# Kernel tuning notes

Hardware: AMD Instinct MI355X
Metric: run time of the kernel (lower is better)

The kernel has to match this reference:

```python
import jax, jax.numpy as jnp
import numpy as np

B, T, D, H, K = 8, 4096, 768, 12, 64
EPS_WKV = 1e-9
EPS_GN = 1e-5


def setup_inputs() -> dict:
    key = jax.random.key(0)
    ks = jax.random.split(key, 12)
    x = jax.random.normal(ks[0], (B, T, D), jnp.float32)
    # linear projection weights (torch nn.Linear stores [out, in]; y = x @ W.T)
    W_r = jax.random.normal(ks[1], (D, D), jnp.float32) * 0.02
    W_k = jax.random.normal(ks[2], (D, D), jnp.float32) * 0.02
    W_v = jax.random.normal(ks[3], (D, D), jnp.float32) * 0.02
    W_o = jax.random.normal(ks[4], (D, D), jnp.float32) * 0.02
    time_mix_r = jax.random.uniform(ks[5], (D,), jnp.float32)
    time_mix_k = jax.random.uniform(ks[6], (D,), jnp.float32)
    time_mix_v = jax.random.uniform(ks[7], (D,), jnp.float32)
    # around the module's init values (time_decay ~ -0.075, time_first ~ 0.15 at layer 6/12)
    time_decay = -0.075 + 0.1 * jax.random.normal(ks[8], (H, K), jnp.float32)
    time_first = 0.15 + 0.1 * jax.random.normal(ks[9], (H, K), jnp.float32)
    gn_weight = jnp.ones((D,), jnp.float32)
    gn_bias = jnp.zeros((D,), jnp.float32)
    return {
        "x": x,
        "time_mix_r": time_mix_r, "time_mix_k": time_mix_k, "time_mix_v": time_mix_v,
        "time_decay": time_decay, "time_first": time_first,
        "W_r": W_r, "W_k": W_k, "W_v": W_v, "W_o": W_o,
        "gn_weight": gn_weight, "gn_bias": gn_bias,
    }


def reference(x, time_mix_r, time_mix_k, time_mix_v, time_decay, time_first,
              W_r, W_k, W_v, W_o, gn_weight, gn_bias):
    Bx, Tx, Dx = x.shape
    Hx, Kx = time_decay.shape
    # token-shift: previous timestep (zero-initialized state)
    x_prev = jnp.concatenate([jnp.zeros_like(x[:, :1]), x[:, :-1]], axis=1)
    xr = x * time_mix_r + x_prev * (1.0 - time_mix_r)
    xk = x * time_mix_k + x_prev * (1.0 - time_mix_k)
    xv = x * time_mix_v + x_prev * (1.0 - time_mix_v)
    r = jax.nn.sigmoid(xr @ W_r.T).reshape(Bx, Tx, Hx, Kx)
    k = (xk @ W_k.T).reshape(Bx, Tx, Hx, Kx)
    v = (xv @ W_v.T).reshape(Bx, Tx, Hx, Kx)

    w = jnp.exp(-jnp.exp(time_decay))   # [H,K] decay per channel
    eu = jnp.exp(time_first)            # [H,K] bonus for current token

    def step(carry, kv_t):
        num, den = carry                # each [B,H,K]
        k_t, v_t = kv_t                 # each [B,H,K]
        ek = jnp.exp(k_t)
        wkv = (num + eu * ek * v_t) / (den + eu * ek + EPS_WKV)
        return (num * w + ek * v_t, den * w + ek), wkv

    k_tm = jnp.moveaxis(k, 1, 0)        # [T,B,H,K]
    v_tm = jnp.moveaxis(v, 1, 0)
    init = (jnp.zeros((Bx, Hx, Kx), x.dtype), jnp.zeros((Bx, Hx, Kx), x.dtype))
    _, wkv = jax.lax.scan(step, init, (k_tm, v_tm))
    out = jnp.moveaxis(wkv, 0, 1)       # [B,T,H,K]

    y = r * out                         # [B,T,H,K]
    # torch GroupNorm(H, D) on [B, D, T]: normalize each group over (K channels x T steps)
    mean = y.mean(axis=(1, 3), keepdims=True)
    var = y.var(axis=(1, 3), keepdims=True)
    y = (y - mean) * jax.lax.rsqrt(var + EPS_GN)
    y = y * gn_weight.reshape(1, 1, Hx, Kx) + gn_bias.reshape(1, 1, Hx, Kx)
    return y.reshape(Bx, Tx, Dx) @ W_o.T
```

## Files before the change

kernel.cpp:

```cpp
#include <hip/hip_runtime.h>
#include <hip/hip_bf16.h>
#include <cstdint>

#define B_ 8
#define T_ 4096
#define D_ 768
#define H_ 12
#define M_ (B_*T_)
#define CHUNKS 256
#define CLEN 16
#define WELEM (D_*D_)
#define NCH (B_*H_*64)

typedef __attribute__((ext_vector_type(8))) short bf16x8;
typedef __attribute__((ext_vector_type(4))) float f32x4;

static __device__ __forceinline__ unsigned short f2bf(float f) {
  __hip_bfloat16 h = __float2bfloat16(f);
  return __builtin_bit_cast(unsigned short, h);
}
static __device__ __forceinline__ float bf2f(unsigned short u) {
  unsigned v = ((unsigned)u) << 16;
  return __builtin_bit_cast(float, v);
}

static __device__ __forceinline__ void async16(const void* g, void* l) {
  __builtin_amdgcn_global_load_lds(
      (const __attribute__((address_space(1))) unsigned int*)g,
      (__attribute__((address_space(3))) unsigned int*)l, 16, 0, 0);
}

__global__ __launch_bounds__(256) void zero_out_kernel(float* __restrict__ out, size_t n4) {
  size_t gid = (size_t)blockIdx.x * 256 + threadIdx.x;
  if (gid < n4) *(float4*)(out + gid * 4) = make_float4(0.f, 0.f, 0.f, 0.f);
}

__global__ __launch_bounds__(256) void mix_kernel(
    const float* __restrict__ x, const float* __restrict__ tmr,
    const float* __restrict__ tmk, const float* __restrict__ tmv,
    unsigned short* __restrict__ xr, unsigned short* __restrict__ xk,
    unsigned short* __restrict__ xv) {
  size_t gid = (size_t)blockIdx.x * 256 + threadIdx.x;
  size_t idx4 = gid * 4;
  int d = (int)(idx4 % D_);
  size_t row = idx4 / D_;
  int t = (int)(row & (T_ - 1));
  float4 xc = *(const float4*)(x + idx4);
  float4 xp = make_float4(0.f, 0.f, 0.f, 0.f);
  if (t > 0) xp = *(const float4*)(x + idx4 - D_);
  float4 mr = *(const float4*)(tmr + d);
  float4 mk = *(const float4*)(tmk + d);
  float4 mv = *(const float4*)(tmv + d);
  ushort4 orr, okk, ovv;
  orr.x = f2bf(xc.x*mr.x + xp.x*(1.f-mr.x));
  orr.y = f2bf(xc.y*mr.y + xp.y*(1.f-mr.y));
  orr.z = f2bf(xc.z*mr.z + xp.z*(1.f-mr.z));
  orr.w = f2bf(xc.w*mr.w + xp.w*(1.f-mr.w));
  okk.x = f2bf(xc.x*mk.x + xp.x*(1.f-mk.x));
  okk.y = f2bf(xc.y*mk.y + xp.y*(1.f-mk.y));
  okk.z = f2bf(xc.z*mk.z + xp.z*(1.f-mk.z));
  okk.w = f2bf(xc.w*mk.w + xp.w*(1.f-mk.w));
  ovv.x = f2bf(xc.x*mv.x + xp.x*(1.f-mv.x));
  ovv.y = f2bf(xc.y*mv.y + xp.y*(1.f-mv.y));
  ovv.z = f2bf(xc.z*mv.z + xp.z*(1.f-mv.z));
  ovv.w = f2bf(xc.w*mv.w + xp.w*(1.f-mv.w));
  *(ushort4*)(xr + idx4) = orr;
  *(ushort4*)(xk + idx4) = okk;
  *(ushort4*)(xv + idx4) = ovv;
}

__global__ __launch_bounds__(256) void wconv_kernel(
    const float* __restrict__ a, const float* __restrict__ b,
    const float* __restrict__ c, const float* __restrict__ d,
    unsigned short* __restrict__ o) {
  size_t gid = (size_t)blockIdx.x * 256 + threadIdx.x;
  size_t idx4 = gid * 4;
  size_t mi = idx4 / WELEM;
  size_t off = idx4 % WELEM;
  const float* src = (mi == 0) ? a : (mi == 1) ? b : (mi == 2) ? c : d;
  float4 v = *(const float4*)(src + off);
  ushort4 u;
  u.x = f2bf(v.x); u.y = f2bf(v.y); u.z = f2bf(v.z); u.w = f2bf(v.w);
  *(ushort4*)(o + idx4) = u;
}

template<int ACT, int OBF>
__global__ __launch_bounds__(256) void gemm_nt(
    const unsigned short* __restrict__ A,
    const unsigned short* __restrict__ Bw,
    void* __restrict__ Cv, int M, int N, int Kd) {
  __shared__ __align__(16) unsigned short smem[128 * 128];
  unsigned short* As = smem;
  unsigned short* Bs = smem + 128 * 64;
  const int tid = threadIdx.x;
  const int wave = tid >> 6, lane = tid & 63;
  const int quad = lane >> 4, l16 = lane & 15;

  int nwg = gridDim.x * gridDim.y;
  int lin = blockIdx.y * gridDim.x + blockIdx.x;
  int q = nwg >> 3, r = nwg & 7;
  int xcd = lin & 7, off = lin >> 3;
  int swz = (xcd < r ? xcd * (q + 1) : r * (q + 1) + (xcd - r) * q) + off;
  const int m0 = (swz / gridDim.x) * 128;
  const int n0 = (swz % gridDim.x) * 128;
  const int wm = (wave & 1) * 64, wn = (wave >> 1) * 64;

  f32x4 acc[4][4] = {};

  for (int kb = 0; kb < Kd; kb += 64) {
    __syncthreads();
#pragma unroll
    for (int j = 0; j < 4; ++j) {
      int chunk = j * 256 + tid;
      int row = chunk >> 3, slot = chunk & 7;
      int ks = slot ^ (row & 7);
      async16(A  + ((size_t)(m0 + row) * Kd + kb + ks * 8), &As[chunk * 8]);
      async16(Bw + ((size_t)(n0 + row) * Kd + kb + ks * 8), &Bs[chunk * 8]);
    }
    __syncthreads();

#pragma unroll
    for (int kk = 0; kk < 2; ++kk) {
      bf16x8 a[4], b[4];
#pragma unroll
      for (int i = 0; i < 4; ++i) {
        int ra = wm + i * 16 + l16;
        a[i] = *(const bf16x8*)&As[ra * 64 + (((kk * 4 + quad) ^ (ra & 7)) * 8)];
        int rb = wn + i * 16 + l16;
        b[i] = *(const bf16x8*)&Bs[rb * 64 + (((kk * 4 + quad) ^ (rb & 7)) * 8)];
      }
#pragma unroll
      for (int i = 0; i < 4; ++i)
#pragma unroll
        for (int jj = 0; jj < 4; ++jj)
          acc[i][jj] = __builtin_amdgcn_mfma_f32_16x16x32_bf16(a[i], b[jj], acc[i][jj], 0, 0, 0);
    }
  }

  if (OBF) {
    __syncthreads();
    unsigned short* Cs = smem;
#pragma unroll
    for (int i = 0; i < 4; ++i) {
#pragma unroll
      for (int jj = 0; jj < 4; ++jj) {
        int col = wn + jj * 16 + l16;
#pragma unroll
        for (int rr = 0; rr < 4; ++rr) {
          int row = wm + i * 16 + quad * 4 + rr;
          float v = acc[i][jj][rr];
          if (ACT == 1) v = 1.f / (1.f + __expf(-v));
          int cg = (col >> 3) ^ (row & 7);
          Cs[row * 128 + cg * 8 + (col & 7)] = f2bf(v);
        }
      }
    }
    __syncthreads();
#pragma unroll
    for (int g = 0; g < 8; ++g) {
      int gi = g * 256 + tid;
      int row = gi >> 4, cg = gi & 15;
      int sg = cg ^ (row & 7);
      bf16x8 vv = *(const bf16x8*)&Cs[row * 128 + sg * 8];
      *(bf16x8*)((unsigned short*)Cv + (size_t)(m0 + row) * N + n0 + cg * 8) = vv;
    }
  } else {
#pragma unroll
    for (int i = 0; i < 4; ++i) {
      int rowb = m0 + wm + i * 16 + quad * 4;
#pragma unroll
      for (int jj = 0; jj < 4; ++jj) {
        int col = n0 + wn + jj * 16 + l16;
#pragma unroll
        for (int rr = 0; rr < 4; ++rr) {
          float v = acc[i][jj][rr];
          ((float*)Cv)[(size_t)(rowb + rr) * N + col] = v;
        }
      }
    }
  }
}

__global__ __launch_bounds__(256) void wkv_pass1(
    const unsigned short* __restrict__ Kb, const unsigned short* __restrict__ Vb,
    const float* __restrict__ td,
    float* __restrict__ sumN, float* __restrict__ sumD) {
  int gid = blockIdx.x * 256 + threadIdx.x;
  int kg = gid & 7;
  int tmp = gid >> 3;
  int h = tmp % H_;
  tmp /= H_;
  int b = tmp % B_;
  int c = tmp / B_;
  const float* tdp = td + h * 64 + kg * 8;
  float w[8], num[8], den[8];
#pragma unroll
  for (int j = 0; j < 8; ++j) {
    w[j] = __expf(-__expf(tdp[j]));
    num[j] = 0.f; den[j] = 0.f;
  }
  size_t base = ((size_t)(b * T_ + c * CLEN)) * D_ + h * 64 + kg * 8;
#pragma unroll 4
  for (int i = 0; i < CLEN; ++i) {
    bf16x8 k8 = *(const bf16x8*)(Kb + base + (size_t)i * D_);
    bf16x8 v8 = *(const bf16x8*)(Vb + base + (size_t)i * D_);
#pragma unroll
    for (int j = 0; j < 8; ++j) {
      float ek = __expf(bf2f((unsigned short)k8[j]));
      num[j] = num[j] * w[j] + ek * bf2f((unsigned short)v8[j]);
      den[j] = den[j] * w[j] + ek;
    }
  }
  int ob = ((c * B_ + b) * H_ + h) * 64 + kg * 8;
  *(float4*)(sumN + ob)     = make_float4(num[0], num[1], num[2], num[3]);
  *(float4*)(sumN + ob + 4) = make_float4(num[4], num[5], num[6], num[7]);
  *(float4*)(sumD + ob)     = make_float4(den[0], den[1], den[2], den[3]);
  *(float4*)(sumD + ob + 4) = make_float4(den[4], den[5], den[6], den[7]);
}

__global__ __launch_bounds__(256) void wkv_pass2(
    const float* __restrict__ sumN, const float* __restrict__ sumD,
    const float* __restrict__ td,
    float* __restrict__ prefN, float* __restrict__ prefD,
    float* __restrict__ gstats) {
  int tid = blockIdx.x * 256 + threadIdx.x;
  if (blockIdx.x == 0 && threadIdx.x < 192) gstats[threadIdx.x] = 0.f;
  int k = tid & 63;
  int h = (tid >> 6) % H_;
  float w = __expf(-__expf(td[h * 64 + k]));
  float wL = w;
#pragma unroll
  for (int i = 0; i < 4; ++i) wL *= wL;
  float n = 0.f, d = 0.f;
  for (int c = 0; c < CHUNKS; ++c) {
    int j = c * NCH + tid;
    prefN[j] = n; prefD[j] = d;
    n = n * wL + sumN[j];
    d = d * wL + sumD[j];
  }
}

__global__ __launch_bounds__(256) void wkv_pass3(
    const unsigned short* __restrict__ Kb, const unsigned short* __restrict__ Vb,
    unsigned short* __restrict__ RY,
    const float* __restrict__ td, const float* __restrict__ tf,
    const float* __restrict__ prefN, const float* __restrict__ prefD,
    float* __restrict__ gsum, float* __restrict__ gsq) {
  int gid = blockIdx.x * 256 + threadIdx.x;
  int kg = gid & 7;
  int tmp = gid >> 3;
  int h = tmp % H_;
  tmp /= H_;
  int b = tmp % B_;
  int c = tmp / B_;
  const float* tdp = td + h * 64 + kg * 8;
  const float* tfp = tf + h * 64 + kg * 8;
  float w[8], eu[8], num[8], den[8];
  int sb = ((c * B_ + b) * H_ + h) * 64 + kg * 8;
  float4 n0 = *(const float4*)(prefN + sb), n1 = *(const float4*)(prefN + sb + 4);
  float4 d0 = *(const float4*)(prefD + sb), d1 = *(const float4*)(prefD + sb + 4);
  num[0]=n0.x; num[1]=n0.y; num[2]=n0.z; num[3]=n0.w;
  num[4]=n1.x; num[5]=n1.y; num[6]=n1.z; num[7]=n1.w;
  den[0]=d0.x; den[1]=d0.y; den[2]=d0.z; den[3]=d0.w;
  den[4]=d1.x; den[5]=d1.y; den[6]=d1.z; den[7]=d1.w;
#pragma unroll
  for (int j = 0; j < 8; ++j) {
    w[j]  = __expf(-__expf(tdp[j]));
    eu[j] = __expf(tfp[j]);
  }
  size_t base = ((size_t)(b * T_ + c * CLEN)) * D_ + h * 64 + kg * 8;
  float s1 = 0.f, s2 = 0.f;
#pragma unroll 4
  for (int i = 0; i < CLEN; ++i) {
    size_t idx = base + (size_t)i * D_;
    bf16x8 k8 = *(const bf16x8*)(Kb + idx);
    bf16x8 v8 = *(const bf16x8*)(Vb + idx);
    bf16x8 r8 = *(const bf16x8*)(RY + idx);
    bf16x8 y8;
#pragma unroll
    for (int j = 0; j < 8; ++j) {
      float kk = bf2f((unsigned short)k8[j]);
      float vv = bf2f((unsigned short)v8[j]);
      float rr = bf2f((unsigned short)r8[j]);
      float ek = __expf(kk);
      float wkv = (num[j] + eu[j] * ek * vv) / (den[j] + eu[j] * ek + 1e-9f);
      unsigned short ybf = f2bf(rr * wkv);
      y8[j] = (short)ybf;
      float y = bf2f(ybf);
      s1 += y; s2 += y * y;
      num[j] = num[j] * w[j] + ek * vv;
      den[j] = den[j] * w[j] + ek;
    }
    *(bf16x8*)(RY + idx) = y8;
  }
#pragma unroll
  for (int off = 4; off; off >>= 1) {
    s1 += __shfl_xor(s1, off);
    s2 += __shfl_xor(s2, off);
  }
  if (kg == 0) {
    atomicAdd(&gsum[b * H_ + h], s1);
    atomicAdd(&gsq [b * H_ + h], s2);
  }
}

__global__ __launch_bounds__(256) void gn_kernel(
    const unsigned short* __restrict__ Y, const float* __restrict__ gsum,
    const float* __restrict__ gsq, const float* __restrict__ gw,
    const float* __restrict__ gb, unsigned short* __restrict__ Ybf) {
  size_t gid = (size_t)blockIdx.x * 256 + threadIdx.x;
  size_t idx4 = gid * 4;
  int d = (int)(idx4 % D_);
  size_t row = idx4 / D_;
  int b = (int)(row >> 12);
  int h = d >> 6;
  int g = b * H_ + h;
  const float inv = 1.f / (float)(T_ * 64);
  float mean = gsum[g] * inv;
  float var = gsq[g] * inv - mean * mean;
  float rstd = rsqrtf(var + 1e-5f);
  ushort4 yu = *(const ushort4*)(Y + idx4);
  float4 wv = *(const float4*)(gw + d);
  float4 bv = *(const float4*)(gb + d);
  ushort4 o;
  o.x = f2bf((bf2f(yu.x) - mean) * rstd * wv.x + bv.x);
  o.y = f2bf((bf2f(yu.y) - mean) * rstd * wv.y + bv.y);
  o.z = f2bf((bf2f(yu.z) - mean) * rstd * wv.z + bv.z);
  o.w = f2bf((bf2f(yu.w) - mean) * rstd * wv.w + bv.w);
  *(ushort4*)(Ybf + idx4) = o;
}

extern "C" void kernel_launch(void* const* d_in, const int* in_sizes, int n_in,
                              void* d_out, int out_size, void* d_ws, size_t ws_size,
                              hipStream_t stream) {
  (void)in_sizes; (void)n_in;
  const float* x   = (const float*)d_in[0];
  const float* tmr = (const float*)d_in[1];
  const float* tmk = (const float*)d_in[2];
  const float* tmv = (const float*)d_in[3];
  const float* td  = (const float*)d_in[4];
  const float* tf  = (const float*)d_in[5];
  const float* Wr  = (const float*)d_in[6];
  const float* Wk  = (const float*)d_in[7];
  const float* Wv  = (const float*)d_in[8];
  const float* Wo  = (const float*)d_in[9];
  const float* gw  = (const float*)d_in[10];
  const float* gb  = (const float*)d_in[11];
  float* out = (float*)d_out;

  constexpr size_t MD = (size_t)M_ * D_;
  constexpr size_t NEED = 4 * (MD * 2)
                        + (size_t)4 * WELEM * 2
                        + 4 * ((size_t)CHUNKS * NCH * 4)
                        + 1024;
  if (ws_size < NEED) {
    zero_out_kernel<<<(int)((MD / 4 + 255) / 256), 256, 0, stream>>>(out, MD / 4);
    return;
  }

  char* ws = (char*)d_ws;
  unsigned short* XR = (unsigned short*)ws; ws += MD * 2;
  unsigned short* XK = (unsigned short*)ws; ws += MD * 2;
  unsigned short* XV = (unsigned short*)ws; ws += MD * 2;
  unsigned short* Rb = (unsigned short*)ws; ws += MD * 2;
  unsigned short* Wb = (unsigned short*)ws; ws += (size_t)4 * WELEM * 2;
  float* sumN  = (float*)ws; ws += (size_t)CHUNKS * NCH * 4;
  float* sumD  = (float*)ws; ws += (size_t)CHUNKS * NCH * 4;
  float* prefN = (float*)ws; ws += (size_t)CHUNKS * NCH * 4;
  float* prefD = (float*)ws; ws += (size_t)CHUNKS * NCH * 4;
  float* gstats = (float*)ws; ws += 1024;
  unsigned short* Kb = XR;
  unsigned short* Vb = XK;
  unsigned short* Yb = XV;

  mix_kernel<<<(int)(MD / 1024), 256, 0, stream>>>(x, tmr, tmk, tmv, XR, XK, XV);
  wconv_kernel<<<(4 * WELEM / 4) / 256, 256, 0, stream>>>(Wr, Wk, Wv, Wo, Wb);

  dim3 ggrid(D_ / 128, M_ / 128);
  gemm_nt<1, 1><<<ggrid, 256, 0, stream>>>(XR, Wb,             Rb, M_, D_, D_);
  gemm_nt<0, 1><<<ggrid, 256, 0, stream>>>(XK, Wb + WELEM,     Kb, M_, D_, D_);
  gemm_nt<0, 1><<<ggrid, 256, 0, stream>>>(XV, Wb + 2 * WELEM, Vb, M_, D_, D_);

  wkv_pass1<<<(CHUNKS * NCH / 8) / 256, 256, 0, stream>>>(Kb, Vb, td, sumN, sumD);
  wkv_pass2<<<NCH / 256, 256, 0, stream>>>(sumN, sumD, td, prefN, prefD, gstats);
  wkv_pass3<<<(CHUNKS * NCH / 8) / 256, 256, 0, stream>>>(Kb, Vb, Rb, td, tf,
                                                          prefN, prefD, gstats, gstats + 96);
  gn_kernel<<<(int)(MD / 1024), 256, 0, stream>>>(Rb, gstats, gstats + 96, gw, gb, Yb);

  gemm_nt<0, 0><<<ggrid, 256, 0, stream>>>(Yb, Wb + 3 * WELEM, out, M_, D_, D_);
}
```

Measured before the change: 538.3 us.

## Multi-stage pipeline GEMM loads, parallelize chunk prefix scan, use fast divide

Result: no change. 538.6 us (+0.1%).

```diff
diff --git a/kernel.cpp b/kernel.cpp
--- a/kernel.cpp
+++ b/kernel.cpp
@@ -89,9 +89,7 @@
     const unsigned short* __restrict__ A,
     const unsigned short* __restrict__ Bw,
     void* __restrict__ Cv, int M, int N, int Kd) {
-  __shared__ __align__(16) unsigned short smem[128 * 128];
-  unsigned short* As = smem;
-  unsigned short* Bs = smem + 128 * 64;
+  __shared__ __align__(16) unsigned short smem[4][128 * 64];
   const int tid = threadIdx.x;
   const int wave = tid >> 6, lane = tid & 63;
   const int quad = lane >> 4, l16 = lane & 15;
@@ -105,41 +103,48 @@
   const int n0 = (swz % gridDim.x) * 128;
   const int wm = (wave & 1) * 64, wn = (wave >> 1) * 64;
 
-  f32x4 acc[4][4] = {};
-
-  for (int kb = 0; kb < Kd; kb += 64) {
-    __syncthreads();
-#pragma unroll
-    for (int j = 0; j < 4; ++j) {
+  auto stage = [&](int buf, int kb) {
+    unsigned short* As = smem[buf];
+    unsigned short* Bs = smem[buf] + 128 * 32;
+#pragma unroll
+    for (int j = 0; j < 2; ++j) {
       int chunk = j * 256 + tid;
-      int row = chunk >> 3, slot = chunk & 7;
-      int ks = slot ^ (row & 7);
+      int row = chunk >> 2, slot = chunk & 3;
+      int ks = slot ^ ((row >> 1) & 3);
       async16(A  + ((size_t)(m0 + row) * Kd + kb + ks * 8), &As[chunk * 8]);
       async16(Bw + ((size_t)(n0 + row) * Kd + kb + ks * 8), &Bs[chunk * 8]);
     }
-    __syncthreads();
-
-#pragma unroll
-    for (int kk = 0; kk < 2; ++kk) {
-      bf16x8 a[4], b[4];
-#pragma unroll
-      for (int i = 0; i < 4; ++i) {
-        int ra = wm + i * 16 + l16;
-        a[i] = *(const bf16x8*)&As[ra * 64 + (((kk * 4 + quad) ^ (ra & 7)) * 8)];
-        int rb = wn + i * 16 + l16;
-        b[i] = *(const bf16x8*)&Bs[rb * 64 + (((kk * 4 + quad) ^ (rb & 7)) * 8)];
-      }
-#pragma unroll
-      for (int i = 0; i < 4; ++i)
-#pragma unroll
-        for (int jj = 0; jj < 4; ++jj)
-          acc[i][jj] = __builtin_amdgcn_mfma_f32_16x16x32_bf16(a[i], b[jj], acc[i][jj], 0, 0, 0);
-    }
+  };
+
+  f32x4 acc[4][4] = {};
+  const int NT = Kd >> 5;
+
+  stage(0, 0); stage(1, 32); stage(2, 64);
+  for (int t = 0; t < NT; ++t) {
+    if (t < NT - 2)       asm volatile("s_waitcnt vmcnt(8)" ::: "memory");
+    else if (t == NT - 2) asm volatile("s_waitcnt vmcnt(4)" ::: "memory");
+    else                  asm volatile("s_waitcnt vmcnt(0)" ::: "memory");
+    __builtin_amdgcn_s_barrier();
+    if (t + 3 < NT) stage((t + 3) & 3, (t + 3) * 32);
+    const unsigned short* As = smem[t & 3];
+    const unsigned short* Bs = smem[t & 3] + 128 * 32;
+    bf16x8 a[4], b[4];
+#pragma unroll
+    for (int i = 0; i < 4; ++i) {
+      int ra = wm + i * 16 + l16;
+      a[i] = *(const bf16x8*)&As[ra * 32 + ((quad ^ ((ra >> 1) & 3)) * 8)];
+      int rb = wn + i * 16 + l16;
+      b[i] = *(const bf16x8*)&Bs[rb * 32 + ((quad ^ ((rb >> 1) & 3)) * 8)];
+    }
+#pragma unroll
+    for (int i = 0; i < 4; ++i)
+#pragma unroll
+      for (int jj = 0; jj < 4; ++jj)
+        acc[i][jj] = __builtin_amdgcn_mfma_f32_16x16x32_bf16(a[i], b[jj], acc[i][jj], 0, 0, 0);
   }
 
   if (OBF) {
-    __syncthreads();
-    unsigned short* Cs = smem;
+    unsigned short* Cs = (unsigned short*)smem;
 #pragma unroll
     for (int i = 0; i < 4; ++i) {
 #pragma unroll
@@ -223,20 +228,49 @@
     const float* __restrict__ td,
     float* __restrict__ prefN, float* __restrict__ prefD,
     float* __restrict__ gstats) {
-  int tid = blockIdx.x * 256 + threadIdx.x;
-  if (blockIdx.x == 0 && threadIdx.x < 192) gstats[threadIdx.x] = 0.f;
-  int k = tid & 63;
-  int h = (tid >> 6) % H_;
-  float w = __expf(-__expf(td[h * 64 + k]));
+  __shared__ float tile[256][64];
+  int bid = blockIdx.x;
+  if (bid == 0 && threadIdx.x < 192) gstats[threadIdx.x] = 0.f;
+  int bh = bid >> 1, qd = bid & 1;
+  const float* src = qd ? sumD : sumN;
+  float* dst = qd ? prefD : prefN;
+  int h = bh % H_;
+  int base = bh * 64;
+  int t = threadIdx.x;
+  {
+    int c4 = (t & 15) * 4;
+    int rg = t >> 4;
+#pragma unroll 4
+    for (int i = 0; i < 16; ++i) {
+      int row = rg * 16 + i;
+      *(float4*)&tile[row][c4] = *(const float4*)&src[(size_t)row * NCH + base + c4];
+    }
+  }
+  __syncthreads();
+  int ch = t & 63, g = t >> 6;
+  float w = __expf(-__expf(td[h * 64 + ch]));
   float wL = w;
 #pragma unroll
   for (int i = 0; i < 4; ++i) wL *= wL;
-  float n = 0.f, d = 0.f;
-  for (int c = 0; c < CHUNKS; ++c) {
-    int j = c * NCH + tid;
-    prefN[j] = n; prefD[j] = d;
-    n = n * wL + sumN[j];
-    d = d * wL + sumD[j];
+  float v = 0.f;
+  for (int i = 0; i < 64; ++i) {
+    int row = g * 64 + i;
+    v = v * wL + tile[row][ch];
+    tile[row][ch] = v;
+  }
+  __syncthreads();
+  float wL64 = wL;
+#pragma unroll
+  for (int i = 0; i < 6; ++i) wL64 *= wL64;
+  float E = 0.f;
+  for (int gp = 0; gp < g; ++gp)
+    E = E * wL64 + tile[gp * 64 + 63][ch];
+  float f = 1.f;
+  for (int i = 0; i < 64; ++i) {
+    int row = g * 64 + i;
+    float P = (i == 0) ? E : tile[row - 1][ch] + E * f;
+    dst[(size_t)row * NCH + base + ch] = P;
+    f *= wL;
   }
 }
 
@@ -283,7 +317,7 @@
       float vv = bf2f((unsigned short)v8[j]);
       float rr = bf2f((unsigned short)r8[j]);
       float ek = __expf(kk);
-      float wkv = (num[j] + eu[j] * ek * vv) / (den[j] + eu[j] * ek + 1e-9f);
+      float wkv = __fdividef(num[j] + eu[j] * ek * vv, den[j] + eu[j] * ek + 1e-9f);
       unsigned short ybf = f2bf(rr * wkv);
       y8[j] = (short)ybf;
       float y = bf2f(ybf);
@@ -382,7 +416,7 @@
   gemm_nt<0, 1><<<ggrid, 256, 0, stream>>>(XV, Wb + 2 * WELEM, Vb, M_, D_, D_);
 
   wkv_pass1<<<(CHUNKS * NCH / 8) / 256, 256, 0, stream>>>(Kb, Vb, td, sumN, sumD);
-  wkv_pass2<<<NCH / 256, 256, 0, stream>>>(sumN, sumD, td, prefN, prefD, gstats);
+  wkv_pass2<<<192, 256, 0, stream>>>(sumN, sumD, td, prefN, prefD, gstats);
   wkv_pass3<<<(CHUNKS * NCH / 8) / 256, 256, 0, stream>>>(Kb, Vb, Rb, td, tf,
                                                           prefN, prefD, gstats, gstats + 96);
   gn_kernel<<<(int)(MD / 1024), 256, 0, stream>>>(Rb, gstats, gstats + 96, gw, gb, Yb);
```
